# Kernel tuning notes

Hardware: AMD Instinct MI355X
Metric: run time of the kernel (lower is better)

## Reference

```python
import jax, jax.numpy as jnp
import numpy as np

HEADS = 8
DIM_HEAD = 32
EPS = 1e-5


def setup_inputs() -> dict:
    key = jax.random.key(0)
    ks = jax.random.split(key, 12)
    b, dim, H, W = 16, 256, 64, 64
    led = 128
    hid = HEADS * DIM_HEAD
    return {
        "x": jax.random.normal(ks[0], (b, dim, H, W), dtype=jnp.float32),
        "condition": jax.random.normal(ks[1], (b, led), dtype=jnp.float32),
        "w_qkv": jax.random.normal(ks[2], (3 * hid, dim), dtype=jnp.float32) * 0.02,
        "w_lk": jax.random.normal(ks[3], (hid, led), dtype=jnp.float32) * 0.02,
        "b_lk": jax.random.normal(ks[4], (hid,), dtype=jnp.float32) * 0.02,
        "w_lq": jax.random.normal(ks[5], (hid, led), dtype=jnp.float32) * 0.02,
        "b_lq": jax.random.normal(ks[6], (hid,), dtype=jnp.float32) * 0.02,
        "w_out": jax.random.normal(ks[7], (dim, hid), dtype=jnp.float32) * 0.02,
        "b_out": jax.random.normal(ks[8], (dim,), dtype=jnp.float32) * 0.02,
        "gn_gamma": jnp.ones((dim,), dtype=jnp.float32),
        "gn_beta": jnp.zeros((dim,), dtype=jnp.float32),
    }


def reference(x, condition, w_qkv, w_lk, b_lk, w_lq, b_lq, w_out, b_out, gn_gamma, gn_beta):
    b, c, H, W = x.shape
    n = H * W
    scale = DIM_HEAD ** (-0.5)
    hid = HEADS * DIM_HEAD

    # 1x1 conv QKV projection (no bias)
    qkv = jnp.einsum('oc,bchw->bohw', w_qkv, x)  # [b, 3*hid, H, W]
    qkv = qkv.reshape(b, 3, HEADS, DIM_HEAD, n)
    q, k, v = qkv[:, 0], qkv[:, 1], qkv[:, 2]     # each [b, heads, d, n]

    # conditioning biases
    lk = (condition @ w_lk.T + b_lk).reshape(b, HEADS, DIM_HEAD, 1)
    lq = (condition @ w_lq.T + b_lq).reshape(b, HEADS, DIM_HEAD, 1)
    k = k + lk
    q = q + lq

    # double softmax (linear attention)
    q = jax.nn.softmax(q, axis=-2) * scale  # over feature dim d
    k = jax.nn.softmax(k, axis=-1)          # over spatial dim n

    context = jnp.einsum('bhdn,bhen->bhde', k, v)   # [b, h, d, e]
    out = jnp.einsum('bhde,bhdn->bhen', context, q)  # [b, h, e, n]
    out = out.reshape(b, hid, H, W)

    # to_out: 1x1 conv + bias, then GroupNorm(1, dim)
    y = jnp.einsum('oc,bchw->bohw', w_out, out) + b_out[None, :, None, None]
    mean = jnp.mean(y, axis=(1, 2, 3), keepdims=True)
    var = jnp.var(y, axis=(1, 2, 3), keepdims=True)
    y = (y - mean) * jax.lax.rsqrt(var + EPS)
    return y * gn_gamma[None, :, None, None] + gn_beta[None, :, None, None]
```

## Files before the change

kernel.cpp:

```cpp
#include <hip/hip_runtime.h>
#include <hip/hip_fp8.h>


#define NB    16
#define DIM   256
#define NSP   4096
#define LED   128
#define HID   256
#define NHEAD 8
#define SCALE 0.17677669529663687f

typedef __bf16 bf16x8 __attribute__((ext_vector_type(8)));
typedef float f32x4 __attribute__((ext_vector_type(4)));
typedef unsigned short us8 __attribute__((ext_vector_type(8)));
typedef unsigned short us4 __attribute__((ext_vector_type(4)));

__device__ __forceinline__ unsigned short f2bf(float f){
  unsigned u = __builtin_bit_cast(unsigned, f);
  u += 0x7fffu + ((u >> 16) & 1u);
  return (unsigned short)(u >> 16);
}
__device__ __forceinline__ float bf2f(unsigned short h){
  unsigned u = ((unsigned)h) << 16;
  return __builtin_bit_cast(float, u);
}
__device__ __forceinline__ unsigned char f2e4m3(float f){
  __hip_fp8_e4m3 h(f);
  return (unsigned char)h.__x;
}
__device__ __forceinline__ float e4m32f(unsigned char c){
  __hip_fp8_e4m3 h;
  h.__x = (__hip_fp8_storage_t)c;
  return (float)h;
}
__device__ __forceinline__ bf16x8 ldb8(const unsigned short* p){
  us8 r = *(const us8*)p;
  return __builtin_bit_cast(bf16x8, r);
}
__device__ __forceinline__ f32x4 mfma16(bf16x8 a, bf16x8 b, f32x4 c){
  return __builtin_amdgcn_mfma_f32_16x16x32_bf16(a, b, c, 0, 0, 0);
}
__device__ __forceinline__ f32x4 mfma8(long a, long b, f32x4 c){
  return __builtin_amdgcn_mfma_f32_16x16x32_fp8_fp8(a, b, c, 0, 0, 0);
}
__device__ __forceinline__ void gl16(const unsigned short* g, unsigned short* l){
  __builtin_amdgcn_global_load_lds(
      (const __attribute__((address_space(1))) unsigned int*)g,
      (__attribute__((address_space(3))) unsigned int*)l,
      16, 0, 0);
}

__global__ __launch_bounds__(256) void k0_prep(
    const float* __restrict__ wqkv, const float* __restrict__ cond,
    const float* __restrict__ wlk, const float* __restrict__ blk,
    const float* __restrict__ wlq, const float* __restrict__ blq,
    unsigned short* __restrict__ whi,
    float* __restrict__ lk, float* __restrict__ lq)
{
  const int idx = blockIdx.x*256 + threadIdx.x;
  if (idx < 768*256){
    whi[idx] = f2bf(wqkv[idx]);
  } else {
    int i = idx - 768*256;
    const int which = (i >= NB*HID) ? 1 : 0;
    i &= (NB*HID - 1);
    const int b = i >> 8, o = i & 255;
    const float* wm = which ? wlq : wlk;
    const float* bs = which ? blq : blk;
    float s = bs[o];
    const float* c = cond + b*LED;
    const float* wr = wm + o*LED;
    for (int j=0;j<LED;j++) s += c[j]*wr[j];
    (which ? lq : lk)[i] = s;
  }
}

__global__ __launch_bounds__(256) void k1_txpose(
    const float* __restrict__ x, unsigned short* __restrict__ xt)
{
  __shared__ float tile[64][65];
  const int c0 = blockIdx.x*64, n0 = blockIdx.y*64, b = blockIdx.z;
  const int t = threadIdx.x;
  const int tr = t >> 6, tc = t & 63;
  const float* xp = x + ((size_t)b*DIM + c0)*NSP + n0;
  #pragma unroll
  for (int i=0;i<16;i++){
    const int cl = i*4 + tr;
    tile[cl][tc] = xp[(size_t)cl*NSP + tc];
  }
  __syncthreads();
  unsigned short* xtp = xt + ((size_t)b*NSP + n0)*DIM + c0;
  #pragma unroll
  for (int pass=0; pass<2; pass++){
    const int nl = pass*32 + (t>>3);
    const int c8 = (t&7)*8;
    us8 v;
    #pragma unroll
    for (int j=0;j<8;j++) v[j] = f2bf(tile[c8+j][nl]);
    *(us8*)&xtp[(size_t)nl*DIM + c8] = v;
  }
}

__global__ __launch_bounds__(256) void k2_gemm1(
    const unsigned short* __restrict__ whi,
    const unsigned short* __restrict__ xt,
    const float* __restrict__ lkv, const float* __restrict__ lqv,
    unsigned short* __restrict__ qh,
    unsigned char* __restrict__ kexp, unsigned char* __restrict__ vout,
    float* __restrict__ ksum)
{
  __shared__ __align__(16) unsigned char smraw[32768];
  unsigned short* Ah   = (unsigned short*)smraw;
  unsigned short* Bt   = (unsigned short*)(smraw + 16384);
  unsigned short* stg  = (unsigned short*)smraw;
  unsigned char*  stg8 = (unsigned char*)smraw;

  const int nt = blockIdx.x, mt = blockIdx.y, b = blockIdx.z;
  const int o0 = mt*128, n0 = nt*128;
  const int t = threadIdx.x, lane = t & 63, wv = t >> 6;
  const int wr = wv >> 1, wc = wv & 1;
  const int cl = lane & 15, g = lane >> 4;

  f32x4 acc[4][4];
  const f32x4 z4 = {0.f,0.f,0.f,0.f};
  #pragma unroll
  for (int m=0;m<4;m++)
    #pragma unroll
    for (int n=0;n<4;n++) acc[m][n] = z4;

  const unsigned short* xb = xt + ((size_t)b*NSP + n0)*DIM;
  const int rowc = lane >> 3;
  const int gcol = 8*((lane & 7) ^ rowc);

  for (int kt=0; kt<4; kt++){
    const int k0 = kt*64;
    __syncthreads();
    #pragma unroll
    for (int j=0;j<4;j++){
      const int rg = wv*4 + j;
      const int rr = rg*8 + rowc;
      gl16(&whi[(size_t)(o0+rr)*DIM + k0 + gcol], &Ah[rg*512]);
      gl16(&xb [(size_t)rr*DIM      + k0 + gcol], &Bt[rg*512]);
    }
    __syncthreads();
    #pragma unroll
    for (int kk=0; kk<2; kk++){
      const int ko = kk*32 + g*8;
      const int kosw = ko ^ ((cl & 7) << 3);
      bf16x8 a1[4], bb[4];
      #pragma unroll
      for (int m=0;m<4;m++)
        a1[m] = ldb8(&Ah[(wr*64 + m*16 + cl)*64 + kosw]);
      #pragma unroll
      for (int n=0;n<4;n++)
        bb[n] = ldb8(&Bt[(wc*64 + n*16 + cl)*64 + kosw]);
      #pragma unroll
      for (int m=0;m<4;m++)
        #pragma unroll
        for (int n=0;n<4;n++)
          acc[m][n] = mfma16(a1[m], bb[n], acc[m][n]);
    }
  }

  __syncthreads();

  if (mt < 2){
    float lqr[4][4];
    #pragma unroll
    for (int m=0;m<4;m++)
      #pragma unroll
      for (int i=0;i<4;i++)
        lqr[m][i] = lqv[b*HID + o0 + wr*64 + m*16 + g*4 + i];
    #pragma unroll
    for (int j=0;j<2;j++){
      #pragma unroll
      for (int nf=0;nf<4;nf++){
        float e[8]; float mx = -1e30f;
        #pragma unroll
        for (int mm=0;mm<2;mm++)
          #pragma unroll
          for (int i=0;i<4;i++){
            const int m = 2*j+mm;
            const float v = acc[m][nf][i] + lqr[m][i];
            e[mm*4+i] = v; mx = fmaxf(mx, v);
          }
        mx = fmaxf(mx, __shfl_xor(mx, 16));
        mx = fmaxf(mx, __shfl_xor(mx, 32));
        float s = 0.f;
        #pragma unroll
        for (int q2=0;q2<8;q2++){ e[q2] = __expf(e[q2]-mx); s += e[q2]; }
        s += __shfl_xor(s, 16);
        s += __shfl_xor(s, 32);
        const float r = 1.f/s;
        const int n_local = wc*64 + nf*16 + cl;
        const int rsw = (n_local & 7) << 3;
        #pragma unroll
        for (int mm=0;mm<2;mm++){
          const int dg_local = wr*64 + (2*j+mm)*16 + g*4;
          us4 h4;
          #pragma unroll
          for (int i=0;i<4;i++) h4[i] = f2bf(e[mm*4+i]*r);
          *(us4*)&stg[n_local*128 + (dg_local ^ rsw)] = h4;
        }
      }
    }
    __syncthreads();
    unsigned short* qbase = qh + ((size_t)b*NSP + n0)*HID + o0;
    #pragma unroll
    for (int i2=0;i2<8;i2++){
      const int n_local = wv*32 + i2*4 + (lane>>4);
      const int dg8 = (lane&15)*8;
      us8 val = *(const us8*)&stg[n_local*128 + (dg8 ^ ((n_local&7)<<3))];
      *(us8*)&qbase[(size_t)n_local*HID + dg8] = val;
    }
  } else {
    const int isK = (mt < 4);
    const int dgbase = isK ? (mt-2)*128 : (mt-4)*128;
    #pragma unroll
    for (int m=0;m<4;m++)
      #pragma unroll
      for (int i=0;i<4;i++){
        const int dg_local = wr*64 + m*16 + g*4 + i;
        const int nb0 = wc*64 + cl;
        if (isK){
          const float lkval = lkv[b*HID + dgbase + dg_local];
          float s = 0.f;
          #pragma unroll
          for (int nf=0;nf<4;nf++){
            const float v = __expf(acc[m][nf][i] + lkval);
            const unsigned char c8v = f2e4m3(v);
            stg8[dg_local*144 + nb0 + nf*16] = c8v;
            s += e4m32f(c8v);
          }
          s += __shfl_xor(s,1); s += __shfl_xor(s,2);
          s += __shfl_xor(s,4); s += __shfl_xor(s,8);
          if (cl == 0) atomicAdd(&ksum[b*HID + dgbase + dg_local], s);
        } else {
          #pragma unroll
          for (int nf=0;nf<4;nf++)
            stg8[dg_local*144 + nb0 + nf*16] = f2e4m3(acc[m][nf][i]);
        }
      }
    __syncthreads();
    unsigned char* obase = (isK ? kexp : vout) + ((size_t)b*HID + dgbase)*NSP + n0;
    const int lane8 = t & 7;
    const int rowid = t >> 3;
    #pragma unroll
    for (int i2=0;i2<4;i2++){
      const int dg_local = i2*32 + rowid;
      us8 val = *(const us8*)&stg8[dg_local*144 + lane8*16];
      *(us8*)&obase[(size_t)dg_local*NSP + lane8*16] = val;
    }
  }
}

__global__ __launch_bounds__(256) void k3_ctx(
    const unsigned char* __restrict__ kexp, const unsigned char* __restrict__ vv,
    float* __restrict__ ctxp)
{
  const int half = blockIdx.x, h = blockIdx.y, b = blockIdx.z;
  const int t = threadIdx.x, lane = t&63, wv = t>>6;
  const int cl = lane&15, g = lane>>4;
  const int nstart = half*2048 + wv*512;
  f32x4 acc[2][2];
  const f32x4 z4 = {0.f,0.f,0.f,0.f};
  acc[0][0]=z4; acc[0][1]=z4; acc[1][0]=z4; acc[1][1]=z4;
  const unsigned char* kb = kexp + ((size_t)b*HID + h*32)*NSP;
  const unsigned char* vb = vv   + ((size_t)b*HID + h*32)*NSP;
  for (int ks=0; ks<16; ks++){
    const int k = nstart + ks*32 + g*8;
    long a0 = *(const long*)&kb[(size_t)(cl)   *NSP + k];
    long a1 = *(const long*)&kb[(size_t)(16+cl)*NSP + k];
    long b0 = *(const long*)&vb[(size_t)(cl)   *NSP + k];
    long b1 = *(const long*)&vb[(size_t)(16+cl)*NSP + k];
    acc[0][0] = mfma8(a0,b0,acc[0][0]);
    acc[0][1] = mfma8(a0,b1,acc[0][1]);
    acc[1][0] = mfma8(a1,b0,acc[1][0]);
    acc[1][1] = mfma8(a1,b1,acc[1][1]);
  }
  float* outp = ctxp + ((((size_t)b*NHEAD + h)*2 + half)*4 + wv)*1024;
  #pragma unroll
  for (int dm=0;dm<2;dm++)
    #pragma unroll
    for (int em=0;em<2;em++)
      #pragma unroll
      for (int i=0;i<4;i++)
        outp[(dm*16 + g*4 + i)*32 + em*16 + cl] = acc[dm][em][i];
}

__global__ __launch_bounds__(256) void k4_m(
    const float* __restrict__ ctxp, const float* __restrict__ ksum,
    const float* __restrict__ wout,
    unsigned short* __restrict__ mhi)
{
  const int h = blockIdx.x, b = blockIdx.y;
  __shared__ float ctxl[32][32];
  __shared__ float rkn[32];
  const int t = threadIdx.x;
  const float* base = ctxp + (((size_t)b*NHEAD + h)*8)*1024;
  #pragma unroll
  for (int r=0;r<4;r++){
    const int de = r*256 + t;
    float s = 0.f;
    #pragma unroll
    for (int p=0;p<8;p++) s += base[p*1024 + de];
    ctxl[de>>5][de&31] = s;
  }
  if (t < 32) rkn[t] = SCALE / ksum[b*HID + h*32 + t];
  __syncthreads();
  float w[32];
  const float* wrow = wout + (size_t)t*HID + h*32;
  #pragma unroll
  for (int el=0;el<32;el++) w[el] = wrow[el];
  for (int dl=0; dl<32; dl++){
    float s = 0.f;
    #pragma unroll
    for (int el=0;el<32;el++) s += w[el]*ctxl[dl][el];
    s *= rkn[dl];
    mhi[((size_t)b*HID + t)*HID + h*32 + dl] = f2bf(s);
  }
}

__global__ __launch_bounds__(256) void k5a_stats(
    const unsigned short* __restrict__ mhi,
    const unsigned short* __restrict__ qhp, const float* __restrict__ bout,
    float* __restrict__ bsum, float* __restrict__ bssq)
{
  __shared__ __align__(16) unsigned char smraw[32768];
  unsigned short* Ah = (unsigned short*)smraw;
  unsigned short* Bh = (unsigned short*)(smraw + 16384);
  __shared__ float red[8];

  const int nt = blockIdx.x, mt = blockIdx.y, b = blockIdx.z;
  const int o0 = mt*128, n0 = nt*128;
  const int t = threadIdx.x, lane = t&63, wv = t>>6;
  const int wr = wv>>1, wc = wv&1;
  const int cl = lane&15, g = lane>>4;

  f32x4 acc[4][4];
  const f32x4 z4 = {0.f,0.f,0.f,0.f};
  #pragma unroll
  for (int m=0;m<4;m++)
    #pragma unroll
    for (int n=0;n<4;n++) acc[m][n] = z4;

  const unsigned short* ab_h = mhi + (size_t)b*HID*HID;
  const unsigned short* bb_h = qhp + ((size_t)b*NSP + n0)*HID;
  const int rowc = lane >> 3;
  const int gcol = 8*((lane & 7) ^ rowc);

  for (int kt=0; kt<4; kt++){
    const int k0 = kt*64;
    __syncthreads();
    #pragma unroll
    for (int j=0;j<4;j++){
      const int rg = wv*4 + j;
      const int rr = rg*8 + rowc;
      gl16(&ab_h[(size_t)(o0+rr)*HID + k0 + gcol], &Ah[rg*512]);
      gl16(&bb_h[(size_t)rr*HID      + k0 + gcol], &Bh[rg*512]);
    }
    __syncthreads();
    #pragma unroll
    for (int kk=0;kk<2;kk++){
      const int ko = kk*32 + g*8;
      const int kosw = ko ^ ((cl & 7) << 3);
      bf16x8 ah[4], bh[4];
      #pragma unroll
      for (int m=0;m<4;m++)
        ah[m] = ldb8(&Ah[(wr*64 + m*16 + cl)*64 + kosw]);
      #pragma unroll
      for (int n=0;n<4;n++)
        bh[n] = ldb8(&Bh[(wc*64 + n*16 + cl)*64 + kosw]);
      #pragma unroll
      for (int m=0;m<4;m++)
        #pragma unroll
        for (int n=0;n<4;n++)
          acc[m][n] = mfma16(ah[m], bh[n], acc[m][n]);
    }
  }

  float lsum = 0.f, lss = 0.f;
  #pragma unroll
  for (int m=0;m<4;m++)
    #pragma unroll
    for (int i=0;i<4;i++){
      const float bo = bout[o0 + wr*64 + m*16 + g*4 + i];
      #pragma unroll
      for (int nf=0;nf<4;nf++){
        const float v = acc[m][nf][i] + bo;
        lsum += v; lss += v*v;
      }
    }
  #pragma unroll
  for (int sft=1; sft<64; sft<<=1){
    lsum += __shfl_xor(lsum, sft);
    lss  += __shfl_xor(lss,  sft);
  }
  if (lane == 0){ red[wv] = lsum; red[4+wv] = lss; }
  __syncthreads();
  if (t == 0){
    atomicAdd(&bsum[b], red[0]+red[1]+red[2]+red[3]);
    atomicAdd(&bssq[b], red[4]+red[5]+red[6]+red[7]);
  }
}

__global__ __launch_bounds__(256) void k5b_write(
    const unsigned short* __restrict__ mhi,
    const unsigned short* __restrict__ qhp, const float* __restrict__ bout,
    const float* __restrict__ bsum, const float* __restrict__ bssq,
    const float* __restrict__ gamma, const float* __restrict__ beta,
    float* __restrict__ out)
{
  __shared__ __align__(16) unsigned char smraw[32768];
  unsigned short* Ah = (unsigned short*)smraw;
  unsigned short* Bh = (unsigned short*)(smraw + 16384);
  float* stg = (float*)smraw;

  const int nt = blockIdx.x, mt = blockIdx.y, b = blockIdx.z;
  const int o0 = mt*128, n0 = nt*128;
  const int t = threadIdx.x, lane = t&63, wv = t>>6;
  const int wr = wv>>1, wc = wv&1;
  const int cl = lane&15, g = lane>>4;

  f32x4 acc[4][4];
  const f32x4 z4 = {0.f,0.f,0.f,0.f};
  #pragma unroll
  for (int m=0;m<4;m++)
    #pragma unroll
    for (int n=0;n<4;n++) acc[m][n] = z4;

  const unsigned short* ab_h = mhi + (size_t)b*HID*HID;
  const unsigned short* bb_h = qhp + ((size_t)b*NSP + n0)*HID;
  const int rowc = lane >> 3;
  const int gcol = 8*((lane & 7) ^ rowc);

  for (int kt=0; kt<4; kt++){
    const int k0 = kt*64;
    __syncthreads();
    #pragma unroll
    for (int j=0;j<4;j++){
      const int rg = wv*4 + j;
      const int rr = rg*8 + rowc;
      gl16(&ab_h[(size_t)(o0+rr)*HID + k0 + gcol], &Ah[rg*512]);
      gl16(&bb_h[(size_t)rr*HID      + k0 + gcol], &Bh[rg*512]);
    }
    __syncthreads();
    #pragma unroll
    for (int kk=0;kk<2;kk++){
      const int ko = kk*32 + g*8;
      const int kosw = ko ^ ((cl & 7) << 3);
      bf16x8 ah[4], bh[4];
      #pragma unroll
      for (int m=0;m<4;m++)
        ah[m] = ldb8(&Ah[(wr*64 + m*16 + cl)*64 + kosw]);
      #pragma unroll
      for (int n=0;n<4;n++)
        bh[n] = ldb8(&Bh[(wc*64 + n*16 + cl)*64 + kosw]);
      #pragma unroll
      for (int m=0;m<4;m++)
        #pragma unroll
        for (int n=0;n<4;n++)
          acc[m][n] = mfma16(ah[m], bh[n], acc[m][n]);
    }
  }

  const float inv = 1.f/1048576.f;
  const float mean = bsum[b]*inv;
  const float var  = bssq[b]*inv - mean*mean;
  const float ri = rsqrtf(var + 1e-5f);
  float gav[4][4], bev[4][4];
  #pragma unroll
  for (int m=0;m<4;m++)
    #pragma unroll
    for (int i=0;i<4;i++){
      const int o = o0 + wr*64 + m*16 + g*4 + i;
      const float ga = gamma[o]*ri;
      gav[m][i] = ga;
      bev[m][i] = beta[o] + (bout[o]-mean)*ga;
    }

  #pragma unroll
  for (int p=0;p<2;p++){
    __syncthreads();
    #pragma unroll
    for (int mm=0;mm<2;mm++){
      const int m = 2*p+mm;
      #pragma unroll
      for (int nf=0;nf<4;nf++)
        #pragma unroll
        for (int i=0;i<4;i++){
          const int lr = wr*32 + mm*16 + g*4 + i;
          const int col = wc*64 + nf*16 + cl;
          stg[lr*128 + (col ^ ((lr&7)<<2))] = acc[m][nf][i]*gav[m][i] + bev[m][i];
        }
    }
    __syncthreads();
    #pragma unroll
    for (int i2=0;i2<8;i2++){
      const int lr = wv*16 + i2*2 + (lane>>5);
      const int colw = (lane&31)*4;
      f32x4 v = *(const f32x4*)&stg[lr*128 + (colw ^ ((lr&7)<<2))];
      const int dg = o0 + (lr>>5)*64 + p*32 + (lr&31);
      *(f32x4*)&out[((size_t)b*HID + dg)*NSP + n0 + colw] = v;
    }
  }
}

#define OFF_XT     0ull
#define OFF_QH     33554432ull
#define OFF_CTXP   67108864ull
#define OFF_MH     71303168ull
#define OFF_LK     73400320ull
#define OFF_LQ     73416704ull
#define OFF_WHI    73433088ull
#define OFF_KSUM   73826304ull
#define OFF_BSUM   73842688ull
#define OFF_BSSQ   73842752ull

extern "C" void kernel_launch(void* const* d_in, const int* in_sizes, int n_in,
                              void* d_out, int out_size, void* d_ws, size_t ws_size,
                              hipStream_t stream) {
  const float* x     = (const float*)d_in[0];
  const float* cond  = (const float*)d_in[1];
  const float* wqkv  = (const float*)d_in[2];
  const float* wlk   = (const float*)d_in[3];
  const float* blk   = (const float*)d_in[4];
  const float* wlq   = (const float*)d_in[5];
  const float* blq   = (const float*)d_in[6];
  const float* wout  = (const float*)d_in[7];
  const float* bout  = (const float*)d_in[8];
  const float* gamma = (const float*)d_in[9];
  const float* beta  = (const float*)d_in[10];

  char* ws = (char*)d_ws;
  unsigned short* xt   = (unsigned short*)(ws + OFF_XT);
  unsigned short* qh   = (unsigned short*)(ws + OFF_QH);
  float*          ctxp = (float*)(ws + OFF_CTXP);
  unsigned short* mhi  = (unsigned short*)(ws + OFF_MH);
  float*          lk   = (float*)(ws + OFF_LK);
  float*          lq   = (float*)(ws + OFF_LQ);
  unsigned short* whi  = (unsigned short*)(ws + OFF_WHI);
  float*          ksum = (float*)(ws + OFF_KSUM);
  float*          bsum = (float*)(ws + OFF_BSUM);
  float*          bssq = (float*)(ws + OFF_BSSQ);

  unsigned char* kexp = (unsigned char*)d_out;
  unsigned char* vscr = (unsigned char*)d_out + 16777216;
  float*         y    = (float*)d_out;

  hipMemsetAsync(ws + OFF_KSUM, 0, 16384 + 128, stream);

  k0_prep  <<<800, 256, 0, stream>>>(wqkv, cond, wlk, blk, wlq, blq, whi, lk, lq);
  k1_txpose<<<dim3(4,64,16), 256, 0, stream>>>(x, xt);
  k2_gemm1 <<<dim3(32,6,16), 256, 0, stream>>>(whi, xt, lk, lq, qh, kexp, vscr, ksum);
  k3_ctx   <<<dim3(2,8,16), 256, 0, stream>>>(kexp, vscr, ctxp);
  k4_m     <<<dim3(8,16), 256, 0, stream>>>(ctxp, ksum, wout, mhi);
  k5a_stats<<<dim3(32,2,16), 256, 0, stream>>>(mhi, qh, bout, bsum, bssq);
  k5b_write<<<dim3(32,2,16), 256, 0, stream>>>(mhi, qh, bout, bsum, bssq, gamma, beta, y);
}
```

Before: 152.4 us.

## Widen QKV GEMM tile to 256 rows with 512 threads and vectorize prep

The QKV projection kernel now runs 512-thread blocks, each covering 256 output channels by 128 spatial positions. The x tile loaded into LDS is therefore shared across twice as many output rows, which halves B-tile traffic and the number of blocks. Q epilogue staging is split into two halves so that it fits in LDS. The prep kernel vectorizes the bf16 weight conversion and splits each conditioning dot product across four lanes joined by shuffles. The price is fewer blocks in the grid, a larger LDS footprint and extra synchronisation in the Q epilogue.

```diff
diff --git a/kernel.cpp b/kernel.cpp
--- a/kernel.cpp
+++ b/kernel.cpp
@@ -58,20 +58,30 @@
     float* __restrict__ lk, float* __restrict__ lq)
 {
   const int idx = blockIdx.x*256 + threadIdx.x;
-  if (idx < 768*256){
-    whi[idx] = f2bf(wqkv[idx]);
-  } else {
-    int i = idx - 768*256;
-    const int which = (i >= NB*HID) ? 1 : 0;
-    i &= (NB*HID - 1);
-    const int b = i >> 8, o = i & 255;
+  if (idx < 49152){
+    f32x4 w = *(const f32x4*)&wqkv[idx*4];
+    us4 h;
+    #pragma unroll
+    for (int i=0;i<4;i++) h[i] = f2bf(w[i]);
+    *(us4*)&whi[idx*4] = h;
+  } else if (idx < 49152 + 32768){
+    const int i2 = idx - 49152;
+    const int d = i2 >> 2, sub = i2 & 3;
+    const int which = (d >= NB*HID) ? 1 : 0;
+    const int dd = d & (NB*HID - 1);
+    const int b = dd >> 8, o = dd & 255;
     const float* wm = which ? wlq : wlk;
-    const float* bs = which ? blq : blk;
-    float s = bs[o];
     const float* c = cond + b*LED;
     const float* wr = wm + o*LED;
-    for (int j=0;j<LED;j++) s += c[j]*wr[j];
-    (which ? lq : lk)[i] = s;
+    float s = 0.f;
+    #pragma unroll
+    for (int j=0;j<32;j++) s += c[sub*32+j]*wr[sub*32+j];
+    s += __shfl_xor(s, 1);
+    s += __shfl_xor(s, 2);
+    if (sub == 0){
+      const float bias = (which ? blq : blk)[o];
+      (which ? lq : lk)[dd] = s + bias;
+    }
   }
 }
 
@@ -101,7 +111,7 @@
   }
 }
 
-__global__ __launch_bounds__(256) void k2_gemm1(
+__global__ __launch_bounds__(512) void k2_gemm1(
     const unsigned short* __restrict__ whi,
     const unsigned short* __restrict__ xt,
     const float* __restrict__ lkv, const float* __restrict__ lqv,
@@ -109,14 +119,14 @@
     unsigned char* __restrict__ kexp, unsigned char* __restrict__ vout,
     float* __restrict__ ksum)
 {
-  __shared__ __align__(16) unsigned char smraw[32768];
-  unsigned short* Ah   = (unsigned short*)smraw;
-  unsigned short* Bt   = (unsigned short*)(smraw + 16384);
+  __shared__ __align__(16) unsigned char smraw[49152];
+  unsigned short* At   = (unsigned short*)smraw;
+  unsigned short* Bt   = (unsigned short*)(smraw + 32768);
   unsigned short* stg  = (unsigned short*)smraw;
   unsigned char*  stg8 = (unsigned char*)smraw;
 
   const int nt = blockIdx.x, mt = blockIdx.y, b = blockIdx.z;
-  const int o0 = mt*128, n0 = nt*128;
+  const int o0 = mt*256, n0 = nt*128;
   const int t = threadIdx.x, lane = t & 63, wv = t >> 6;
   const int wr = wv >> 1, wc = wv & 1;
   const int cl = lane & 15, g = lane >> 4;
@@ -139,8 +149,13 @@
     for (int j=0;j<4;j++){
       const int rg = wv*4 + j;
       const int rr = rg*8 + rowc;
-      gl16(&whi[(size_t)(o0+rr)*DIM + k0 + gcol], &Ah[rg*512]);
-      gl16(&xb [(size_t)rr*DIM      + k0 + gcol], &Bt[rg*512]);
+      gl16(&whi[(size_t)(o0+rr)*DIM + k0 + gcol], &At[rg*512]);
+    }
+    #pragma unroll
+    for (int j=0;j<2;j++){
+      const int rg = wv*2 + j;
+      const int rr = rg*8 + rowc;
+      gl16(&xb[(size_t)rr*DIM + k0 + gcol], &Bt[rg*512]);
     }
     __syncthreads();
     #pragma unroll
@@ -150,7 +165,7 @@
       bf16x8 a1[4], bb[4];
       #pragma unroll
       for (int m=0;m<4;m++)
-        a1[m] = ldb8(&Ah[(wr*64 + m*16 + cl)*64 + kosw]);
+        a1[m] = ldb8(&At[(wr*64 + m*16 + cl)*64 + kosw]);
       #pragma unroll
       for (int n=0;n<4;n++)
         bb[n] = ldb8(&Bt[(wc*64 + n*16 + cl)*64 + kosw]);
@@ -164,92 +179,96 @@
 
   __syncthreads();
 
-  if (mt < 2){
+  if (mt == 0){
     float lqr[4][4];
     #pragma unroll
     for (int m=0;m<4;m++)
       #pragma unroll
       for (int i=0;i<4;i++)
-        lqr[m][i] = lqv[b*HID + o0 + wr*64 + m*16 + g*4 + i];
-    #pragma unroll
-    for (int j=0;j<2;j++){
-      #pragma unroll
-      for (int nf=0;nf<4;nf++){
-        float e[8]; float mx = -1e30f;
+        lqr[m][i] = lqv[b*HID + wr*64 + m*16 + g*4 + i];
+    #pragma unroll
+    for (int h=0; h<2; h++){
+      if (wc == h){
         #pragma unroll
-        for (int mm=0;mm<2;mm++)
+        for (int j=0;j<2;j++){
           #pragma unroll
-          for (int i=0;i<4;i++){
-            const int m = 2*j+mm;
-            const float v = acc[m][nf][i] + lqr[m][i];
-            e[mm*4+i] = v; mx = fmaxf(mx, v);
+          for (int nf=0;nf<4;nf++){
+            float e[8]; float mx = -1e30f;
+            #pragma unroll
+            for (int mm=0;mm<2;mm++)
+              #pragma unroll
+              for (int i=0;i<4;i++){
+                const int m = 2*j+mm;
+                const float v = acc[m][nf][i] + lqr[m][i];
+                e[mm*4+i] = v; mx = fmaxf(mx, v);
+              }
+            mx = fmaxf(mx, __shfl_xor(mx, 16));
+            mx = fmaxf(mx, __shfl_xor(mx, 32));
+            float s = 0.f;
+            #pragma unroll
+            for (int q2=0;q2<8;q2++){ e[q2] = __expf(e[q2]-mx); s += e[q2]; }
+            s += __shfl_xor(s, 16);
+            s += __shfl_xor(s, 32);
+            const float r = 1.f/s;
+            const int nl = nf*16 + cl;
+            const int rsw = (nl & 7) << 3;
+            #pragma unroll
+            for (int mm=0;mm<2;mm++){
+              const int dg_local = wr*64 + (2*j+mm)*16 + g*4;
+              us4 h4;
+              #pragma unroll
+              for (int i=0;i<4;i++) h4[i] = f2bf(e[mm*4+i]*r);
+              *(us4*)&stg[nl*256 + (dg_local ^ rsw)] = h4;
+            }
           }
-        mx = fmaxf(mx, __shfl_xor(mx, 16));
-        mx = fmaxf(mx, __shfl_xor(mx, 32));
-        float s = 0.f;
-        #pragma unroll
-        for (int q2=0;q2<8;q2++){ e[q2] = __expf(e[q2]-mx); s += e[q2]; }
-        s += __shfl_xor(s, 16);
-        s += __shfl_xor(s, 32);
-        const float r = 1.f/s;
-        const int n_local = wc*64 + nf*16 + cl;
-        const int rsw = (n_local & 7) << 3;
-        #pragma unroll
-        for (int mm=0;mm<2;mm++){
-          const int dg_local = wr*64 + (2*j+mm)*16 + g*4;
-          us4 h4;
-          #pragma unroll
-          for (int i=0;i<4;i++) h4[i] = f2bf(e[mm*4+i]*r);
-          *(us4*)&stg[n_local*128 + (dg_local ^ rsw)] = h4;
         }
       }
-    }
-    __syncthreads();
-    unsigned short* qbase = qh + ((size_t)b*NSP + n0)*HID + o0;
-    #pragma unroll
-    for (int i2=0;i2<8;i2++){
-      const int n_local = wv*32 + i2*4 + (lane>>4);
-      const int dg8 = (lane&15)*8;
-      us8 val = *(const us8*)&stg[n_local*128 + (dg8 ^ ((n_local&7)<<3))];
-      *(us8*)&qbase[(size_t)n_local*HID + dg8] = val;
+      __syncthreads();
+      #pragma unroll
+      for (int it=0; it<4; it++){
+        const int nl = it*16 + (t>>5);
+        const int dg8 = (t&31)*8;
+        us8 val = *(const us8*)&stg[nl*256 + (dg8 ^ ((nl&7)<<3))];
+        *(us8*)&qh[((size_t)b*NSP + n0 + h*64 + nl)*HID + dg8] = val;
+      }
+      __syncthreads();
     }
   } else {
-    const int isK = (mt < 4);
-    const int dgbase = isK ? (mt-2)*128 : (mt-4)*128;
+    const int isK = (mt == 1);
     #pragma unroll
     for (int m=0;m<4;m++)
       #pragma unroll
       for (int i=0;i<4;i++){
-        const int dg_local = wr*64 + m*16 + g*4 + i;
+        const int dg = wr*64 + m*16 + g*4 + i;
         const int nb0 = wc*64 + cl;
         if (isK){
-          const float lkval = lkv[b*HID + dgbase + dg_local];
+          const float lkval = lkv[b*HID + dg];
           float s = 0.f;
           #pragma unroll
           for (int nf=0;nf<4;nf++){
             const float v = __expf(acc[m][nf][i] + lkval);
             const unsigned char c8v = f2e4m3(v);
-            stg8[dg_local*144 + nb0 + nf*16] = c8v;
+            stg8[dg*144 + nb0 + nf*16] = c8v;
             s += e4m32f(c8v);
           }
           s += __shfl_xor(s,1); s += __shfl_xor(s,2);
           s += __shfl_xor(s,4); s += __shfl_xor(s,8);
-          if (cl == 0) atomicAdd(&ksum[b*HID + dgbase + dg_local], s);
+          if (cl == 0) atomicAdd(&ksum[b*HID + dg], s);
         } else {
           #pragma unroll
           for (int nf=0;nf<4;nf++)
-            stg8[dg_local*144 + nb0 + nf*16] = f2e4m3(acc[m][nf][i]);
+            stg8[dg*144 + nb0 + nf*16] = f2e4m3(acc[m][nf][i]);
         }
       }
     __syncthreads();
-    unsigned char* obase = (isK ? kexp : vout) + ((size_t)b*HID + dgbase)*NSP + n0;
+    unsigned char* obase = (isK ? kexp : vout) + ((size_t)b*HID)*NSP + n0;
     const int lane8 = t & 7;
     const int rowid = t >> 3;
     #pragma unroll
     for (int i2=0;i2<4;i2++){
-      const int dg_local = i2*32 + rowid;
-      us8 val = *(const us8*)&stg8[dg_local*144 + lane8*16];
-      *(us8*)&obase[(size_t)dg_local*NSP + lane8*16] = val;
+      const int dg = i2*64 + rowid;
+      us8 val = *(const us8*)&stg8[dg*144 + lane8*16];
+      *(us8*)&obase[(size_t)dg*NSP + lane8*16] = val;
     }
   }
 }
@@ -550,9 +569,9 @@
 
   hipMemsetAsync(ws + OFF_KSUM, 0, 16384 + 128, stream);
 
-  k0_prep  <<<800, 256, 0, stream>>>(wqkv, cond, wlk, blk, wlq, blq, whi, lk, lq);
+  k0_prep  <<<320, 256, 0, stream>>>(wqkv, cond, wlk, blk, wlq, blq, whi, lk, lq);
   k1_txpose<<<dim3(4,64,16), 256, 0, stream>>>(x, xt);
-  k2_gemm1 <<<dim3(32,6,16), 256, 0, stream>>>(whi, xt, lk, lq, qh, kexp, vscr, ksum);
+  k2_gemm1 <<<dim3(32,3,16), 512, 0, stream>>>(whi, xt, lk, lq, qh, kexp, vscr, ksum);
   k3_ctx   <<<dim3(2,8,16), 256, 0, stream>>>(kexp, vscr, ctxp);
   k4_m     <<<dim3(8,16), 256, 0, stream>>>(ctxp, ksum, wout, mhi);
   k5a_stats<<<dim3(32,2,16), 256, 0, stream>>>(mhi, qh, bout, bsum, bssq);
```

After: 149.0 us. -2.2%, faster.
